# Performance work log

Hardware: AMD Instinct MI355X
Metric: run time of the kernel (lower is better)

## Reference

```python
import jax, jax.numpy as jnp
import numpy as np

N, E, D, H, G, C = 50000, 800000, 3, 128, 64, 10

def setup_inputs() -> dict:
    key = jax.random.key(0)
    ks = jax.random.split(key, 10)
    s = 0.1  # small init scale
    return {
        "pos": jax.random.normal(ks[0], (N, D), jnp.float32),
        "edge_index": jax.random.randint(ks[1], (2, E), 0, N, dtype=jnp.int64),
        "batch": jnp.sort(jax.random.randint(ks[2], (N,), 0, G, dtype=jnp.int64)),
        "W1": jax.random.normal(ks[3], (D, H), jnp.float32) * s,
        "b1": jnp.zeros((H,), jnp.float32),
        "W2": jax.random.normal(ks[4], (H, H), jnp.float32) * s,
        "b2": jnp.zeros((H,), jnp.float32),
        "W3": jax.random.normal(ks[5], (H, H), jnp.float32) * s,
        "b3": jnp.zeros((H,), jnp.float32),
        "Wl1": jax.random.normal(ks[6], (H, H // 2), jnp.float32) * s,
        "bl1": jnp.zeros((H // 2,), jnp.float32),
        "Wl2": jax.random.normal(ks[7], (H // 2, C), jnp.float32) * s,
        "bl2": jnp.zeros((C,), jnp.float32),
        "num_graphs": G,
    }

def reference(pos, edge_index, batch, W1, b1, W2, b2, W3, b3, Wl1, bl1, Wl2, bl2, num_graphs):
    n = pos.shape[0]
    loop = jnp.arange(n, dtype=edge_index.dtype)
    # GCN: add self-loops, symmetric normalization deg^-1/2 (A+I) deg^-1/2
    src = jnp.concatenate([edge_index[0], loop])
    dst = jnp.concatenate([edge_index[1], loop])
    deg = jax.ops.segment_sum(jnp.ones(src.shape, pos.dtype), dst, num_segments=n)
    dinv = jax.lax.rsqrt(jnp.maximum(deg, 1e-12))  # deg >= 1 due to self-loops
    norm = dinv[src] * dinv[dst]  # [E+N]

    def gcn(x, W, b):
        h = x @ W                               # [N,F] dense transform first (PyG order)
        msg = h[src] * norm[:, None]            # gather + normalize
        return jax.ops.segment_sum(msg, dst, num_segments=n) + b  # scatter-add

    x = jax.nn.relu(gcn(pos, W1, b1))   # dropout = identity (eval mode)
    x = jax.nn.relu(gcn(x, W2, b2))
    x = jax.nn.relu(gcn(x, W3, b3))
    # global_mean_pool over batch ids
    sums = jax.ops.segment_sum(x, batch, num_segments=num_graphs)
    cnt = jax.ops.segment_sum(jnp.ones((n,), x.dtype), batch, num_segments=num_graphs)
    g = sums / jnp.maximum(cnt, 1.0)[:, None]   # [G,H]
    h = jax.nn.relu(g @ Wl1 + bl1)
    return h @ Wl2 + bl2
```

## Files before the change

### kernel.cpp

```cpp
#include <hip/hip_runtime.h>

#define H 128
#define LSTRIDE 136
typedef unsigned int uint32;
typedef unsigned short ushort16;
typedef __attribute__((ext_vector_type(8))) short bf16x8;
typedef __attribute__((ext_vector_type(4))) float f32x4;

static __device__ __forceinline__ ushort16 f2bf(float f){
  uint32 u = __float_as_uint(f);
  uint32 r = (u + 0x7fff + ((u >> 16) & 1)) >> 16;
  return (ushort16)r;
}
static __device__ __forceinline__ float bflo(uint32 u){ return __uint_as_float(u << 16); }
static __device__ __forceinline__ float bfhi(uint32 u){ return __uint_as_float(u & 0xffff0000u); }

__global__ __launch_bounds__(256) void k_setup(int* __restrict__ deg, float* __restrict__ gsum,
                                               const int* __restrict__ batch, int n, int G,
                                               int* __restrict__ gb){
  int i = blockIdx.x*256 + threadIdx.x;
  if (i < n) deg[i] = 0;
  if (i < G*H) gsum[i] = 0.f;
  if (i <= G){
    int lo = 0, hi = n;
    while (lo < hi){ int m = (lo + hi) >> 1; if (batch[m] < i) lo = m + 1; else hi = m; }
    gb[i] = lo;
  }
}

__global__ __launch_bounds__(256) void k_count_rank(const int* __restrict__ dst, int E,
                                                    int* __restrict__ deg, int* __restrict__ rank){
  int i = blockIdx.x*256 + threadIdx.x;
  if (i < E) rank[i] = atomicAdd(&deg[dst[i]], 1);
}

__global__ __launch_bounds__(256) void k_scan1(const int* __restrict__ deg, int n,
      int* __restrict__ offsets, int* __restrict__ bsum, float* __restrict__ dinv){
  __shared__ int sh[256];
  int b = blockIdx.x, t = threadIdx.x;
  int base = b*1024 + t*4;
  bool i0 = base+0 < n, i1 = base+1 < n, i2 = base+2 < n, i3 = base+3 < n;
  int d0=0,d1=0,d2=0,d3=0;
  if (i3){ int4 v = *(const int4*)&deg[base]; d0=v.x; d1=v.y; d2=v.z; d3=v.w; }
  else {
    if (i0) d0 = deg[base+0];
    if (i1) d1 = deg[base+1];
    if (i2) d2 = deg[base+2];
  }
  int e0 = i0? d0+1:0, e1 = i1? d1+1:0, e2 = i2? d2+1:0, e3 = i3? d3+1:0;
  sh[t] = e0+e1+e2+e3;
  __syncthreads();
  for (int off=1; off<256; off<<=1){
    int v = sh[t];
    int add = (t>=off)? sh[t-off] : 0;
    __syncthreads();
    sh[t] = v+add;
    __syncthreads();
  }
  int o0 = (t==0)?0:sh[t-1];
  int o1 = o0+e0, o2 = o1+e1, o3 = o2+e2;
  if (i0){ offsets[base+0]=o0; dinv[base+0]=rsqrtf((float)(d0+1)); }
  if (i1){ offsets[base+1]=o1; dinv[base+1]=rsqrtf((float)(d1+1)); }
  if (i2){ offsets[base+2]=o2; dinv[base+2]=rsqrtf((float)(d2+1)); }
  if (i3){ offsets[base+3]=o3; dinv[base+3]=rsqrtf((float)(d3+1)); }
  if (t==255) bsum[b] = sh[255];
}

__global__ __launch_bounds__(256) void k_scan3b(int* __restrict__ offsets, int n,
                                                const int* __restrict__ bsum, int B){
  __shared__ int sh[2];
  int b = blockIdx.x, t = threadIdx.x;
  if (t < 64){
    int v   = (t < B)? bsum[t] : 0;
    int pre = (t < b)? v : 0;
    int tot = v;
    for (int o=1; o<64; o<<=1){ pre += __shfl_xor(pre,o); tot += __shfl_xor(tot,o); }
    if (t == 0){ sh[0] = pre; sh[1] = tot; }
  }
  __syncthreads();
  int add = sh[0];
  int base = b*1024 + t*4;
  if (base+3 < n){
    int4 v = *(int4*)&offsets[base];
    v.x+=add; v.y+=add; v.z+=add; v.w+=add;
    *(int4*)&offsets[base] = v;
  } else {
    #pragma unroll
    for (int k=0;k<4;k++){ int i=base+k; if (i<n) offsets[i]+=add; }
  }
  if (b == B-1 && t == 255) offsets[n] = sh[1];
}

__global__ __launch_bounds__(256) void k_fill2(const int* __restrict__ src, const int* __restrict__ dst,
            int E, int n, const int* __restrict__ offsets, const int* __restrict__ rank,
            int* __restrict__ csr_src){
  int i = blockIdx.x*256 + threadIdx.x;
  if (i < E){
    csr_src[offsets[dst[i]] + 1 + rank[i]] = src[i];
  } else if (i < E + n){
    int j = i - E;
    csr_src[offsets[j]] = j;
  }
}

__global__ __launch_bounds__(256) void k_prescale(const float* __restrict__ pos, const float* __restrict__ dinv,
                                                  float4* __restrict__ y0, int n){
  int i = blockIdx.x*256 + threadIdx.x;
  if (i < n){
    float d = dinv[i];
    y0[i] = make_float4(pos[3*i]*d, pos[3*i+1]*d, pos[3*i+2]*d, 0.f);
  }
}

__global__ __launch_bounds__(256) void k_agg3(const float4* __restrict__ y0, const int* __restrict__ offsets,
      const int* __restrict__ csr_src, const float* __restrict__ dinv, float4* __restrict__ a1, int n){
  int node = blockIdx.x*256 + threadIdx.x;
  if (node >= n) return;
  int lo = offsets[node], hi = offsets[node+1];
  float x=0.f, y=0.f, z=0.f;
  int e = lo;
  for (; e+2 <= hi; e += 2){
    int s0 = csr_src[e], s1 = csr_src[e+1];
    float4 v0 = y0[s0], v1 = y0[s1];
    x += v0.x + v1.x; y += v0.y + v1.y; z += v0.z + v1.z;
  }
  if (e < hi){ float4 v = y0[csr_src[e]]; x += v.x; y += v.y; z += v.z; }
  float dn = dinv[node];
  a1[node] = make_float4(x*dn, y*dn, z*dn, 0.f);
}

__global__ __launch_bounds__(128) void k_dense1(const float4* __restrict__ a1, const float* __restrict__ W1,
      const float* __restrict__ b1, const float* __restrict__ dinv, ushort16* __restrict__ y1, int n){
  int node = blockIdx.x;
  if (node >= n) return;
  int f = threadIdx.x;
  float4 v = a1[node];
  float acc = v.x*W1[f] + v.y*W1[H+f] + v.z*W1[2*H+f] + b1[f];
  y1[(size_t)node*H + f] = f2bf(dinv[node] * fmaxf(acc, 0.f));
}

__global__ __launch_bounds__(256) void k_wprep2(const float* __restrict__ W2, const float* __restrict__ W3,
                                                ushort16* __restrict__ wp2, ushort16* __restrict__ wp3){
  int gid = blockIdx.x*256 + threadIdx.x;
  const float* W = (gid < 2048) ? W2 : W3;
  ushort16* wp   = (gid < 2048) ? wp2 : wp3;
  int tid = gid & 2047;
  int frag = tid >> 6, lane = tid & 63;
  int kt = frag >> 3, ct = frag & 7;
  int m = lane & 15, quad = lane >> 4;
  const float* wrow = &W[(kt*32 + quad*8)*H + ct*16 + m];
  ushort16 vals[8];
  #pragma unroll
  for (int j = 0; j < 8; j++) vals[j] = f2bf(wrow[j*H]);
  uint4 o;
  o.x = (uint32)vals[0] | ((uint32)vals[1] << 16);
  o.y = (uint32)vals[2] | ((uint32)vals[3] << 16);
  o.z = (uint32)vals[4] | ((uint32)vals[5] << 16);
  o.w = (uint32)vals[6] | ((uint32)vals[7] << 16);
  *(uint4*)&wp[(size_t)tid*8] = o;
}

template<int BF16OUT>
__global__ __launch_bounds__(256) void k_aggdense(const ushort16* __restrict__ y, const int* __restrict__ offsets,
      const int* __restrict__ csr_src, const float* __restrict__ dinv, const ushort16* __restrict__ wp,
      const float* __restrict__ bias,
      float* __restrict__ xout, ushort16* __restrict__ yout, int n){
  __shared__ unsigned short As[16*LSTRIDE];
  int tid = threadIdx.x;
  int node16 = blockIdx.x*16;
  int nl = tid >> 4;
  int node = node16 + nl;
  int f8 = (tid & 15) * 8;

  float a0=0,a1=0,a2=0,a3=0,a4=0,a5=0,a6=0,a7=0;
  float dn = 0.f;
  #define ADDU(u) { a0+=bflo(u.x); a1+=bfhi(u.x); a2+=bflo(u.y); a3+=bfhi(u.y); \
                    a4+=bflo(u.z); a5+=bfhi(u.z); a6+=bflo(u.w); a7+=bfhi(u.w); }
  if (node < n){
    int lo = offsets[node], hi = offsets[node+1];
    int e = lo;
    for (; e+8 <= hi; e += 8){
      int s0=csr_src[e],   s1=csr_src[e+1], s2=csr_src[e+2], s3=csr_src[e+3];
      int s4=csr_src[e+4], s5=csr_src[e+5], s6=csr_src[e+6], s7=csr_src[e+7];
      uint4 u0 = *(const uint4*)&y[(size_t)s0*H + f8];
      uint4 u1 = *(const uint4*)&y[(size_t)s1*H + f8];
      uint4 u2 = *(const uint4*)&y[(size_t)s2*H + f8];
      uint4 u3 = *(const uint4*)&y[(size_t)s3*H + f8];
      uint4 u4 = *(const uint4*)&y[(size_t)s4*H + f8];
      uint4 u5 = *(const uint4*)&y[(size_t)s5*H + f8];
      uint4 u6 = *(const uint4*)&y[(size_t)s6*H + f8];
      uint4 u7 = *(const uint4*)&y[(size_t)s7*H + f8];
      ADDU(u0); ADDU(u1); ADDU(u2); ADDU(u3);
      ADDU(u4); ADDU(u5); ADDU(u6); ADDU(u7);
    }
    for (; e < hi; e++){
      int s = csr_src[e];
      uint4 u = *(const uint4*)&y[(size_t)s*H + f8];
      ADDU(u);
    }
    dn = dinv[node];
  }
  #undef ADDU
  uint4 o;
  o.x = (uint32)f2bf(a0*dn) | ((uint32)f2bf(a1*dn) << 16);
  o.y = (uint32)f2bf(a2*dn) | ((uint32)f2bf(a3*dn) << 16);
  o.z = (uint32)f2bf(a4*dn) | ((uint32)f2bf(a5*dn) << 16);
  o.w = (uint32)f2bf(a6*dn) | ((uint32)f2bf(a7*dn) << 16);
  *(uint4*)&As[nl*LSTRIDE + f8] = o;
  __syncthreads();

  int wave = tid >> 6;
  int lane = tid & 63;
  int m = lane & 15, quad = lane >> 4;
  f32x4 acc0 = {0.f,0.f,0.f,0.f}, acc1 = {0.f,0.f,0.f,0.f};
  int ct0 = wave*2, ct1 = wave*2 + 1;
  #pragma unroll
  for (int kt = 0; kt < 4; kt++){
    bf16x8 af = *(const bf16x8*)&As[m*LSTRIDE + kt*32 + quad*8];
    bf16x8 b0 = *(const bf16x8*)&wp[(size_t)((kt*8+ct0)*64 + lane)*8];
    bf16x8 b1 = *(const bf16x8*)&wp[(size_t)((kt*8+ct1)*64 + lane)*8];
    acc0 = __builtin_amdgcn_mfma_f32_16x16x32_bf16(af, b0, acc0, 0, 0, 0);
    acc1 = __builtin_amdgcn_mfma_f32_16x16x32_bf16(af, b1, acc1, 0, 0, 0);
  }
  #pragma unroll
  for (int j = 0; j < 2; j++){
    int ct = wave*2 + j;
    int col = ct*16 + m;
    float bv = bias[col];
    f32x4 ac = j ? acc1 : acc0;
    #pragma unroll
    for (int r = 0; r < 4; r++){
      int orow = node16 + quad*4 + r;
      if (orow < n){
        float v = fmaxf(ac[r] + bv, 0.f);
        if (BF16OUT) yout[(size_t)orow*H + col] = f2bf(v * dinv[orow]);
        else         xout[(size_t)orow*H + col] = v;
      }
    }
  }
}

__global__ __launch_bounds__(128) void k_pool_partial(const float* __restrict__ x, const int* __restrict__ gb,
                                                      int S, float* __restrict__ gsum){
  int g = blockIdx.x, s = blockIdx.y;
  int lo = gb[g], hi = gb[g+1];
  int cnt = hi - lo;
  int a = lo + (int)(((long long)cnt * s) / S);
  int b = lo + (int)(((long long)cnt * (s+1)) / S);
  int f = threadIdx.x;
  float acc = 0.f;
  for (int i = a; i < b; i++) acc += x[(size_t)i*H + f];
  if (b > a) atomicAdd(&gsum[g*H + f], acc);
}

__global__ __launch_bounds__(64) void k_head(const float* __restrict__ gsum, const int* __restrict__ gb,
            const float* __restrict__ Wl1, const float* __restrict__ bl1,
            const float* __restrict__ Wl2, const float* __restrict__ bl2,
            float* __restrict__ out){
  int g = blockIdx.x;
  int t = threadIdx.x;
  __shared__ float gs[H];
  __shared__ float h1[64];
  float inv = 1.f / fmaxf((float)(gb[g+1] - gb[g]), 1.f);
  gs[t]      = gsum[g*H + t]      * inv;
  gs[64 + t] = gsum[g*H + 64 + t] * inv;
  __syncthreads();
  float acc = bl1[t];
  for (int k = 0; k < H; k++) acc += gs[k] * Wl1[k*64 + t];
  h1[t] = fmaxf(acc, 0.f);
  __syncthreads();
  if (t < 10){
    float o = bl2[t];
    for (int j = 0; j < 64; j++) o += h1[j] * Wl2[j*10 + t];
    out[g*10 + t] = o;
  }
}

extern "C" void kernel_launch(void* const* d_in, const int* in_sizes, int n_in,
                              void* d_out, int out_size, void* d_ws, size_t ws_size,
                              hipStream_t stream){
  const float* pos = (const float*)d_in[0];
  const int*  ei   = (const int*)d_in[1];
  const int*  batch= (const int*)d_in[2];
  const float* W1 = (const float*)d_in[3];
  const float* b1 = (const float*)d_in[4];
  const float* W2 = (const float*)d_in[5];
  const float* b2 = (const float*)d_in[6];
  const float* W3 = (const float*)d_in[7];
  const float* b3 = (const float*)d_in[8];
  const float* Wl1 = (const float*)d_in[9];
  const float* bl1 = (const float*)d_in[10];
  const float* Wl2 = (const float*)d_in[11];
  const float* bl2 = (const float*)d_in[12];
  float* out = (float*)d_out;

  int N = in_sizes[0] / 3;
  int E = in_sizes[1] / 2;
  int G = out_size / 10;
  const int S = 40;
  int B = (N + 1023) / 1024;

  char* p = (char*)d_ws;
  auto carve = [&](size_t bytes)->char* { char* q = p; p += (bytes + 255) & ~(size_t)255; return q; };
  int*      deg     = (int*)     carve(sizeof(int)    * (size_t)N);
  int*      offsets = (int*)     carve(sizeof(int)    * (size_t)(N+1));
  float*    dinv    = (float*)   carve(sizeof(float)  * (size_t)N);
  int*      bsum    = (int*)     carve(sizeof(int)    * 256);
  int*      gb      = (int*)     carve(sizeof(int)    * (size_t)(G+1));
  float*    gsum    = (float*)   carve(sizeof(float)  * (size_t)G * H);
  int*      csr_src = (int*)     carve(sizeof(int)    * (size_t)(E+N));
  ushort16* ybufB   = (ushort16*)carve(sizeof(ushort16) * (size_t)N * H);
  ushort16* wp2     = (ushort16*)carve(sizeof(ushort16) * 16384);
  ushort16* wp3     = (ushort16*)carve(sizeof(ushort16) * 16384);
  size_t rank_b = (sizeof(int)    * (size_t)E        + 255) & ~(size_t)255;
  size_t y0_b   = (sizeof(float4) * (size_t)N        + 255) & ~(size_t)255;
  size_t a1_b   = (sizeof(float4) * (size_t)N        + 255) & ~(size_t)255;
  size_t ybuf_b = (sizeof(ushort16)* (size_t)N * H   + 255) & ~(size_t)255;
  size_t x3_b   = (sizeof(float)  * (size_t)N * H    + 255) & ~(size_t)255;
  size_t big_b  = rank_b + y0_b + a1_b + ybuf_b;
  if (x3_b > big_b) big_b = x3_b;
  char* big = carve(big_b);
  int*      rank  = (int*)big;
  float4*   y0    = (float4*)(big + rank_b);
  float4*   a1    = (float4*)(big + rank_b + y0_b);
  ushort16* ybufA = (ushort16*)(big + rank_b + y0_b + a1_b);
  float*    x3    = (float*)big;

  const int* src = ei;
  const int* dst = ei + E;

  hipLaunchKernelGGL(k_setup, dim3((N+255)/256), dim3(256), 0, stream, deg, gsum, batch, N, G, gb);

  hipLaunchKernelGGL(k_count_rank, dim3((E+255)/256),   dim3(256), 0, stream, dst, E, deg, rank);
  hipLaunchKernelGGL(k_scan1,      dim3(B),             dim3(256), 0, stream, deg, N, offsets, bsum, dinv);
  hipLaunchKernelGGL(k_scan3b,     dim3(B),             dim3(256), 0, stream, offsets, N, bsum, B);
  hipLaunchKernelGGL(k_fill2,      dim3((E+N+255)/256), dim3(256), 0, stream, src, dst, E, N, offsets, rank, csr_src);

  hipLaunchKernelGGL(k_wprep2, dim3(16), dim3(256), 0, stream, W2, W3, wp2, wp3);

  hipLaunchKernelGGL(k_prescale, dim3((N+255)/256), dim3(256), 0, stream, pos, dinv, y0, N);
  hipLaunchKernelGGL(k_agg3,     dim3((N+255)/256), dim3(256), 0, stream, y0, offsets, csr_src, dinv, a1, N);
  hipLaunchKernelGGL(k_dense1,   dim3(N),           dim3(128), 0, stream, a1, W1, b1, dinv, ybufA, N);

  hipLaunchKernelGGL(k_aggdense<1>, dim3((N+15)/16), dim3(256), 0, stream,
                     ybufA, offsets, csr_src, dinv, wp2, b2, (float*)nullptr, ybufB, N);

  hipLaunchKernelGGL(k_aggdense<0>, dim3((N+15)/16), dim3(256), 0, stream,
                     ybufB, offsets, csr_src, dinv, wp3, b3, x3, (ushort16*)nullptr, N);

  hipLaunchKernelGGL(k_pool_partial, dim3(G, S), dim3(128), 0, stream, x3, gb, S, gsum);
  hipLaunchKernelGGL(k_head,         dim3(G),    dim3(64),  0, stream, gsum, gb, Wl1, bl1, Wl2, bl2, out);
}
```

Measured before the change: 269.1 us.

## Fuse layer-1 aggregate with dense transform and fold mean-pool into layer 3

Merges the 3-wide aggregation and the W1 transform into one per-node kernel that writes bf16 rows directly, removing the a1 buffer and one launch. The last aggregate+MFMA kernel now reduces its 16-row tile per graph in shared memory and atomically adds into the graph sums. This removes the fp32 x3 write and reread and the separate pooling kernel. The cost is more atomics (one per column per graph segment per block) and a layer-1 kernel where each thread writes a full 256-byte row serially.

```diff
diff --git a/kernel.cpp b/kernel.cpp
--- a/kernel.cpp
+++ b/kernel.cpp
@@ -112,8 +112,10 @@
   }
 }
 
-__global__ __launch_bounds__(256) void k_agg3(const float4* __restrict__ y0, const int* __restrict__ offsets,
-      const int* __restrict__ csr_src, const float* __restrict__ dinv, float4* __restrict__ a1, int n){
+__global__ __launch_bounds__(256) void k_layer1(const float4* __restrict__ y0, const int* __restrict__ offsets,
+      const int* __restrict__ csr_src, const float* __restrict__ dinv,
+      const float* __restrict__ W1, const float* __restrict__ b1,
+      ushort16* __restrict__ y1, int n){
   int node = blockIdx.x*256 + threadIdx.x;
   if (node >= n) return;
   int lo = offsets[node], hi = offsets[node+1];
@@ -126,17 +128,32 @@
   }
   if (e < hi){ float4 v = y0[csr_src[e]]; x += v.x; y += v.y; z += v.z; }
   float dn = dinv[node];
-  a1[node] = make_float4(x*dn, y*dn, z*dn, 0.f);
-}
-
-__global__ __launch_bounds__(128) void k_dense1(const float4* __restrict__ a1, const float* __restrict__ W1,
-      const float* __restrict__ b1, const float* __restrict__ dinv, ushort16* __restrict__ y1, int n){
-  int node = blockIdx.x;
-  if (node >= n) return;
-  int f = threadIdx.x;
-  float4 v = a1[node];
-  float acc = v.x*W1[f] + v.y*W1[H+f] + v.z*W1[2*H+f] + b1[f];
-  y1[(size_t)node*H + f] = f2bf(dinv[node] * fmaxf(acc, 0.f));
+  x *= dn; y *= dn; z *= dn;
+  ushort16* rowp = &y1[(size_t)node*H];
+  for (int c8 = 0; c8 < 16; c8++){
+    float4 wa0 = *(const float4*)&W1[c8*8];
+    float4 wa1 = *(const float4*)&W1[c8*8+4];
+    float4 wb0 = *(const float4*)&W1[H + c8*8];
+    float4 wb1 = *(const float4*)&W1[H + c8*8+4];
+    float4 wc0 = *(const float4*)&W1[2*H + c8*8];
+    float4 wc1 = *(const float4*)&W1[2*H + c8*8+4];
+    float4 bb0 = *(const float4*)&b1[c8*8];
+    float4 bb1 = *(const float4*)&b1[c8*8+4];
+    float o0 = fmaxf(x*wa0.x + y*wb0.x + z*wc0.x + bb0.x, 0.f) * dn;
+    float o1 = fmaxf(x*wa0.y + y*wb0.y + z*wc0.y + bb0.y, 0.f) * dn;
+    float o2 = fmaxf(x*wa0.z + y*wb0.z + z*wc0.z + bb0.z, 0.f) * dn;
+    float o3 = fmaxf(x*wa0.w + y*wb0.w + z*wc0.w + bb0.w, 0.f) * dn;
+    float o4 = fmaxf(x*wa1.x + y*wb1.x + z*wc1.x + bb1.x, 0.f) * dn;
+    float o5 = fmaxf(x*wa1.y + y*wb1.y + z*wc1.y + bb1.y, 0.f) * dn;
+    float o6 = fmaxf(x*wa1.z + y*wb1.z + z*wc1.z + bb1.z, 0.f) * dn;
+    float o7 = fmaxf(x*wa1.w + y*wb1.w + z*wc1.w + bb1.w, 0.f) * dn;
+    uint4 o;
+    o.x = (uint32)f2bf(o0) | ((uint32)f2bf(o1) << 16);
+    o.y = (uint32)f2bf(o2) | ((uint32)f2bf(o3) << 16);
+    o.z = (uint32)f2bf(o4) | ((uint32)f2bf(o5) << 16);
+    o.w = (uint32)f2bf(o6) | ((uint32)f2bf(o7) << 16);
+    *(uint4*)&rowp[c8*8] = o;
+  }
 }
 
 __global__ __launch_bounds__(256) void k_wprep2(const float* __restrict__ W2, const float* __restrict__ W3,
@@ -160,17 +177,21 @@
   *(uint4*)&wp[(size_t)tid*8] = o;
 }
 
-template<int BF16OUT>
+template<int POOL>
 __global__ __launch_bounds__(256) void k_aggdense(const ushort16* __restrict__ y, const int* __restrict__ offsets,
       const int* __restrict__ csr_src, const float* __restrict__ dinv, const ushort16* __restrict__ wp,
       const float* __restrict__ bias,
-      float* __restrict__ xout, ushort16* __restrict__ yout, int n){
+      ushort16* __restrict__ yout, const int* __restrict__ batch, float* __restrict__ gsum, int n){
   __shared__ unsigned short As[16*LSTRIDE];
+  __shared__ float pool[POOL ? 16*H : 1];
+  __shared__ int   sbatch[POOL ? 16 : 1];
   int tid = threadIdx.x;
   int node16 = blockIdx.x*16;
   int nl = tid >> 4;
   int node = node16 + nl;
   int f8 = (tid & 15) * 8;
+
+  if (POOL && tid < 16) sbatch[tid] = (node16 + tid < n) ? batch[node16 + tid] : -1;
 
   float a0=0,a1=0,a2=0,a3=0,a4=0,a5=0,a6=0,a7=0;
   float dn = 0.f;
@@ -230,27 +251,32 @@
     f32x4 ac = j ? acc1 : acc0;
     #pragma unroll
     for (int r = 0; r < 4; r++){
-      int orow = node16 + quad*4 + r;
+      int rl = quad*4 + r;
+      int orow = node16 + rl;
       if (orow < n){
         float v = fmaxf(ac[r] + bv, 0.f);
-        if (BF16OUT) yout[(size_t)orow*H + col] = f2bf(v * dinv[orow]);
-        else         xout[(size_t)orow*H + col] = v;
+        if (POOL) pool[rl*H + col] = v;
+        else      yout[(size_t)orow*H + col] = f2bf(v * dinv[orow]);
       }
     }
   }
-}
-
-__global__ __launch_bounds__(128) void k_pool_partial(const float* __restrict__ x, const int* __restrict__ gb,
-                                                      int S, float* __restrict__ gsum){
-  int g = blockIdx.x, s = blockIdx.y;
-  int lo = gb[g], hi = gb[g+1];
-  int cnt = hi - lo;
-  int a = lo + (int)(((long long)cnt * s) / S);
-  int b = lo + (int)(((long long)cnt * (s+1)) / S);
-  int f = threadIdx.x;
-  float acc = 0.f;
-  for (int i = a; i < b; i++) acc += x[(size_t)i*H + f];
-  if (b > a) atomicAdd(&gsum[g*H + f], acc);
+  if (POOL){
+    __syncthreads();
+    if (tid < H){
+      int col = tid;
+      float run = 0.f; int gprev = -1;
+      for (int r = 0; r < 16; r++){
+        int g = sbatch[r];
+        if (g < 0) break;
+        if (g != gprev){
+          if (gprev >= 0) atomicAdd(&gsum[gprev*H + col], run);
+          run = 0.f; gprev = g;
+        }
+        run += pool[r*H + col];
+      }
+      if (gprev >= 0) atomicAdd(&gsum[gprev*H + col], run);
+    }
+  }
 }
 
 __global__ __launch_bounds__(64) void k_head(const float* __restrict__ gsum, const int* __restrict__ gb,
@@ -297,7 +323,6 @@
   int N = in_sizes[0] / 3;
   int E = in_sizes[1] / 2;
   int G = out_size / 10;
-  const int S = 40;
   int B = (N + 1023) / 1024;
 
   char* p = (char*)d_ws;
@@ -309,22 +334,12 @@
   int*      gb      = (int*)     carve(sizeof(int)    * (size_t)(G+1));
   float*    gsum    = (float*)   carve(sizeof(float)  * (size_t)G * H);
   int*      csr_src = (int*)     carve(sizeof(int)    * (size_t)(E+N));
+  int*      rank    = (int*)     carve(sizeof(int)    * (size_t)E);
+  float4*   y0      = (float4*)  carve(sizeof(float4) * (size_t)N);
+  ushort16* ybufA   = (ushort16*)carve(sizeof(ushort16) * (size_t)N * H);
   ushort16* ybufB   = (ushort16*)carve(sizeof(ushort16) * (size_t)N * H);
   ushort16* wp2     = (ushort16*)carve(sizeof(ushort16) * 16384);
   ushort16* wp3     = (ushort16*)carve(sizeof(ushort16) * 16384);
-  size_t rank_b = (sizeof(int)    * (size_t)E        + 255) & ~(size_t)255;
-  size_t y0_b   = (sizeof(float4) * (size_t)N        + 255) & ~(size_t)255;
-  size_t a1_b   = (sizeof(float4) * (size_t)N        + 255) & ~(size_t)255;
-  size_t ybuf_b = (sizeof(ushort16)* (size_t)N * H   + 255) & ~(size_t)255;
-  size_t x3_b   = (sizeof(float)  * (size_t)N * H    + 255) & ~(size_t)255;
-  size_t big_b  = rank_b + y0_b + a1_b + ybuf_b;
-  if (x3_b > big_b) big_b = x3_b;
-  char* big = carve(big_b);
-  int*      rank  = (int*)big;
-  float4*   y0    = (float4*)(big + rank_b);
-  float4*   a1    = (float4*)(big + rank_b + y0_b);
-  ushort16* ybufA = (ushort16*)(big + rank_b + y0_b + a1_b);
-  float*    x3    = (float*)big;
 
   const int* src = ei;
   const int* dst = ei + E;
@@ -339,15 +354,13 @@
   hipLaunchKernelGGL(k_wprep2, dim3(16), dim3(256), 0, stream, W2, W3, wp2, wp3);
 
   hipLaunchKernelGGL(k_prescale, dim3((N+255)/256), dim3(256), 0, stream, pos, dinv, y0, N);
-  hipLaunchKernelGGL(k_agg3,     dim3((N+255)/256), dim3(256), 0, stream, y0, offsets, csr_src, dinv, a1, N);
-  hipLaunchKernelGGL(k_dense1,   dim3(N),           dim3(128), 0, stream, a1, W1, b1, dinv, ybufA, N);
+  hipLaunchKernelGGL(k_layer1,   dim3((N+255)/256), dim3(256), 0, stream, y0, offsets, csr_src, dinv, W1, b1, ybufA, N);
+
+  hipLaunchKernelGGL(k_aggdense<0>, dim3((N+15)/16), dim3(256), 0, stream,
+                     ybufA, offsets, csr_src, dinv, wp2, b2, ybufB, (const int*)nullptr, (float*)nullptr, N);
 
   hipLaunchKernelGGL(k_aggdense<1>, dim3((N+15)/16), dim3(256), 0, stream,
-                     ybufA, offsets, csr_src, dinv, wp2, b2, (float*)nullptr, ybufB, N);
-
-  hipLaunchKernelGGL(k_aggdense<0>, dim3((N+15)/16), dim3(256), 0, stream,
-                     ybufB, offsets, csr_src, dinv, wp3, b3, x3, (ushort16*)nullptr, N);
-
-  hipLaunchKernelGGL(k_pool_partial, dim3(G, S), dim3(128), 0, stream, x3, gb, S, gsum);
-  hipLaunchKernelGGL(k_head,         dim3(G),    dim3(64),  0, stream, gsum, gb, Wl1, bl1, Wl2, bl2, out);
-}
+                     ybufB, offsets, csr_src, dinv, wp3, b3, (ushort16*)nullptr, batch, gsum, N);
+
+  hipLaunchKernelGGL(k_head, dim3(G), dim3(64), 0, stream, gsum, gb, Wl1, bl1, Wl2, bl2, out);
+}
```

New measurement: 262.2 us. 1.03x faster.
